# Kernel optimization log

Hardware: AMD Instinct MI355X
Metric: run time of the kernel (lower is better)

Reference implementation:

```python
import jax, jax.numpy as jnp
import numpy as np

B, C = 8192, 32000


def setup_inputs() -> dict:
    key = jax.random.key(0)
    k1, k2, k3 = jax.random.split(key, 3)
    x = jax.random.normal(k1, (B, C), dtype=jnp.float32)
    y0 = jax.random.randint(k2, (B,), 0, C, dtype=jnp.int64)
    a1_freq = jax.random.uniform(k3, (B,), dtype=jnp.float32)
    return {"x": x, "y0": y0, "a1_freq": a1_freq, "gramma": 1}


def reference(x, y0, a1_freq, gramma):
    # Original: loss = -(1/B) * sum_b (2*a1_freq_b)^gamma * log(exp(x_b[y_b]) / sum(exp(x_b)))
    # i.e. weighted log-softmax NLL, vectorized with a single stable log_softmax.
    logp = jax.nn.log_softmax(x, axis=-1)                      # [B, C]
    picked = jnp.take_along_axis(logp, y0[:, None], axis=-1)[:, 0]  # [B]
    w = (2.0 * a1_freq) ** gramma                              # [B]
    return -jnp.mean(w * picked)
```

## Files before the change

### kernel.cpp

```cpp
#include <hip/hip_runtime.h>
#include <cmath>


__global__ __launch_bounds__(256) void ce_loss_kernel(
    const float* __restrict__ x,
    const int*   __restrict__ y0,
    const float* __restrict__ a1,
    const int*   __restrict__ gramma,
    float*       __restrict__ out,
    int B, int C)
{
    const int row = blockIdx.x;
    const float* xrow = x + (size_t)row * (size_t)C;

    float m = -INFINITY;
    float s = 0.0f;

    auto upd = [&](float v) {
        if (v > m) {
            s = s * __expf(m - v) + 1.0f;
            m = v;
        } else {
            s += __expf(v - m);
        }
    };

    const int n4 = C >> 2;
    const float4* xr4 = reinterpret_cast<const float4*>(xrow);
    for (int i = threadIdx.x; i < n4; i += blockDim.x) {
        float4 v = xr4[i];
        upd(v.x); upd(v.y); upd(v.z); upd(v.w);
    }
    for (int i = (n4 << 2) + threadIdx.x; i < C; i += blockDim.x) {
        upd(xrow[i]);
    }

    #pragma unroll
    for (int off = 32; off >= 1; off >>= 1) {
        float mo = __shfl_down(m, off, 64);
        float so = __shfl_down(s, off, 64);
        float nm = fmaxf(m, mo);
        s = s * __expf(m - nm) + so * __expf(mo - nm);
        m = nm;
    }

    __shared__ float sm[4];
    __shared__ float ss[4];
    const int lane = threadIdx.x & 63;
    const int wid  = threadIdx.x >> 6;
    if (lane == 0) { sm[wid] = m; ss[wid] = s; }
    __syncthreads();

    if (threadIdx.x == 0) {
        float M = sm[0];
        float S = ss[0];
        #pragma unroll
        for (int w = 1; w < 4; ++w) {
            float mo = sm[w], so = ss[w];
            float nm = fmaxf(M, mo);
            S = S * __expf(M - nm) + so * __expf(mo - nm);
            M = nm;
        }
        const float lse = M + logf(S);
        const int   idx = y0[row];
        const float xy  = xrow[idx];
        const float a   = a1[row];
        const int   g   = gramma[0];
        const float w   = (g == 1) ? (2.0f * a) : powf(2.0f * a, (float)g);
        const float contrib = -w * (xy - lse) / (float)B;
        atomicAdd(out, contrib);
    }
}

extern "C" void kernel_launch(void* const* d_in, const int* in_sizes, int n_in,
                              void* d_out, int out_size, void* d_ws, size_t ws_size,
                              hipStream_t stream) {
    const float* x      = (const float*)d_in[0];
    const int*   y0     = (const int*)d_in[1];
    const float* a1     = (const float*)d_in[2];
    const int*   gramma = (const int*)d_in[3];
    float*       out    = (float*)d_out;

    const int B = in_sizes[1];
    const int C = in_sizes[0] / B;

    hipMemsetAsync(out, 0, sizeof(float), stream);
    ce_loss_kernel<<<B, 256, 0, stream>>>(x, y0, a1, gramma, out, B, C);
}
```

Before: 1.302 ms.

## Use unshifted exp-sum with range-checked fallback instead of online softmax

Replaces the per-element online max/rescale update with a plain sum of exp(x) and separate max tracking, using four independent accumulators to break dependency chains. If the row max falls outside [-60, 60], a second pass recomputes the sum shifted by the max. This removes branches and extra exponentials from the hot loop, but relies on inputs being moderate to avoid overflow, and rows outside that range read the data twice.

```diff
diff --git a/kernel.cpp b/kernel.cpp
--- a/kernel.cpp
+++ b/kernel.cpp
@@ -10,58 +10,73 @@
     float*       __restrict__ out,
     int B, int C)
 {
+    constexpr int BS = 256;
     const int row = blockIdx.x;
     const float* xrow = x + (size_t)row * (size_t)C;
 
-    float m = -INFINITY;
-    float s = 0.0f;
-
-    auto upd = [&](float v) {
-        if (v > m) {
-            s = s * __expf(m - v) + 1.0f;
-            m = v;
-        } else {
-            s += __expf(v - m);
-        }
-    };
-
     const int n4 = C >> 2;
     const float4* xr4 = reinterpret_cast<const float4*>(xrow);
-    for (int i = threadIdx.x; i < n4; i += blockDim.x) {
+
+    float m0 = -INFINITY, m1 = -INFINITY, m2 = -INFINITY, m3 = -INFINITY;
+    float s0 = 0.f, s1 = 0.f, s2 = 0.f, s3 = 0.f;
+
+    #pragma unroll 4
+    for (int i = threadIdx.x; i < n4; i += BS) {
         float4 v = xr4[i];
-        upd(v.x); upd(v.y); upd(v.z); upd(v.w);
+        m0 = fmaxf(m0, v.x); s0 += __expf(v.x);
+        m1 = fmaxf(m1, v.y); s1 += __expf(v.y);
+        m2 = fmaxf(m2, v.z); s2 += __expf(v.z);
+        m3 = fmaxf(m3, v.w); s3 += __expf(v.w);
     }
-    for (int i = (n4 << 2) + threadIdx.x; i < C; i += blockDim.x) {
-        upd(xrow[i]);
+    for (int i = (n4 << 2) + threadIdx.x; i < C; i += BS) {
+        float v = xrow[i];
+        m0 = fmaxf(m0, v); s0 += __expf(v);
     }
+
+    float m = fmaxf(fmaxf(m0, m1), fmaxf(m2, m3));
+    float s = (s0 + s1) + (s2 + s3);
 
     #pragma unroll
     for (int off = 32; off >= 1; off >>= 1) {
-        float mo = __shfl_down(m, off, 64);
-        float so = __shfl_down(s, off, 64);
-        float nm = fmaxf(m, mo);
-        s = s * __expf(m - nm) + so * __expf(mo - nm);
-        m = nm;
+        m = fmaxf(m, __shfl_down(m, off, 64));
+        s += __shfl_down(s, off, 64);
     }
 
-    __shared__ float sm[4];
-    __shared__ float ss[4];
+    __shared__ float sm[4], ss[4], bM;
     const int lane = threadIdx.x & 63;
     const int wid  = threadIdx.x >> 6;
     if (lane == 0) { sm[wid] = m; ss[wid] = s; }
     __syncthreads();
 
+    float S = 0.f;
     if (threadIdx.x == 0) {
-        float M = sm[0];
-        float S = ss[0];
+        float M0 = fmaxf(fmaxf(sm[0], sm[1]), fmaxf(sm[2], sm[3]));
+        S = (ss[0] + ss[1]) + (ss[2] + ss[3]);
+        bM = M0;
+    }
+    __syncthreads();
+    const float M = bM;
+    const bool fallback = (M > 60.0f) || (M < -60.0f);
+
+    if (fallback) {
+        float t0 = 0.f, t1 = 0.f, t2 = 0.f, t3 = 0.f;
+        for (int i = threadIdx.x; i < n4; i += BS) {
+            float4 v = xr4[i];
+            t0 += __expf(v.x - M); t1 += __expf(v.y - M);
+            t2 += __expf(v.z - M); t3 += __expf(v.w - M);
+        }
+        for (int i = (n4 << 2) + threadIdx.x; i < C; i += BS)
+            t0 += __expf(xrow[i] - M);
+        float t = (t0 + t1) + (t2 + t3);
         #pragma unroll
-        for (int w = 1; w < 4; ++w) {
-            float mo = sm[w], so = ss[w];
-            float nm = fmaxf(M, mo);
-            S = S * __expf(M - nm) + so * __expf(mo - nm);
-            M = nm;
-        }
-        const float lse = M + logf(S);
+        for (int off = 32; off >= 1; off >>= 1) t += __shfl_down(t, off, 64);
+        if (lane == 0) ss[wid] = t;
+        __syncthreads();
+        if (threadIdx.x == 0) S = (ss[0] + ss[1]) + (ss[2] + ss[3]);
+    }
+
+    if (threadIdx.x == 0) {
+        const float lse = fallback ? (M + logf(S)) : logf(S);
         const int   idx = y0[row];
         const float xy  = xrow[idx];
         const float a   = a1[row];
```

Result: no change. 1.279 ms (-1.8%).
